# Performance work log

Measured on AMD Instinct MI355X. Metric: run time of the kernel, lower is better.

Reference implementation:

```python
import jax, jax.numpy as jnp
import numpy as np

E, C, D, F = 8, 2048, 2048, 8192  # experts, capacity/expert, d_model, d_ff

def setup_inputs() -> dict:
    key = jax.random.key(0)
    ks = jax.random.split(key, 5)
    s_in = 1.0 / np.sqrt(D)
    s_h = 1.0 / np.sqrt(F)
    return {
        "inputs": jax.random.normal(ks[0], (1, E * C, D), dtype=jnp.float32),
        "w1": jax.random.normal(ks[1], (E, D, F), dtype=jnp.float32) * s_in,
        "b1": jax.random.normal(ks[2], (E, F), dtype=jnp.float32) * 0.01,
        "w2": jax.random.normal(ks[3], (E, F, D), dtype=jnp.float32) * s_h,
        "b2": jax.random.normal(ks[4], (E, D), dtype=jnp.float32) * 0.01,
    }

def reference(inputs, w1, b1, w2, b2):
    # inputs: [G, E*C, D]; chunk along dim=1 == reshape to [G, E, C, D]
    G, T, d = inputs.shape
    x = inputs.reshape(G, E, T // E, d)
    # grouped FFN: per-expert Linear -> GELU(exact, torch default) -> Linear
    h = jnp.einsum('gecd,edf->gecf', x, w1) + b1[None, :, None, :]
    h = jax.nn.gelu(h, approximate=False)
    y = jnp.einsum('gecf,efd->gecd', h, w2) + b2[None, :, None, :]
    # torch.cat(expert_outputs, dim=1) == reshape back
    return y.reshape(G, T, d)
```

## Files before the change

kernel.cpp:

```cpp
#include <hip/hip_runtime.h>
#include <hip/hip_bf16.h>


#define E_ 8
#define C_ 2048
#define D_ 2048
#define F_ 8192

typedef short bf16x8 __attribute__((ext_vector_type(8)));
typedef float f32x4  __attribute__((ext_vector_type(4)));

__device__ inline unsigned short f2bf(float f) {
    unsigned u = __float_as_uint(f);
    u += 0x7fffu + ((u >> 16) & 1u);
    return (unsigned short)(u >> 16);
}

__device__ inline float gelu_fast(float x) {
    float z = 0.7978845608028654f * (x + 0.044715f * x * x * x);
    float e = __expf(-2.0f * fabsf(z));
    float t = (1.0f - e) / (1.0f + e);
    t = copysignf(t, z);
    return 0.5f * x * (1.0f + t);
}

__device__ inline void gload_lds16(const void* g, void* l) {
    __builtin_amdgcn_global_load_lds(
        (const __attribute__((address_space(1))) void*)g,
        (__attribute__((address_space(3))) void*)l, 16, 0, 0);
}

__global__ __launch_bounds__(256) void cvt_kernel(
    const float* __restrict__ in, unsigned short* __restrict__ out, long n4)
{
    long i = (long)blockIdx.x * 256 + threadIdx.x;
    if (i >= n4) return;
    float4 v = ((const float4*)in)[i];
    union { unsigned short u[4]; uint2 q; } r;
    r.u[0] = f2bf(v.x); r.u[1] = f2bf(v.y); r.u[2] = f2bf(v.z); r.u[3] = f2bf(v.w);
    ((uint2*)out)[i] = r.q;
}

__global__ __launch_bounds__(256) void transpose_cvt(
    const float* __restrict__ in, unsigned short* __restrict__ out,
    int R, int Cc, int RT, int CT)
{
    __shared__ float lds[64][65];
    int bx = blockIdx.x;
    int e  = bx / (RT * CT);
    int rem = bx % (RT * CT);
    int rt = rem / CT, ct = rem % CT;
    const float* ine = in + (long)e * R * Cc;
    unsigned short* oute = out + (long)e * R * Cc;
    long r0 = (long)rt * 64, c0 = (long)ct * 64;
    int t = threadIdx.x;

    int lr = t >> 4, lc = t & 15;
#pragma unroll
    for (int ii = 0; ii < 4; ++ii) {
        int r = lr + ii * 16;
        float4 v = *(const float4*)(ine + (r0 + r) * Cc + c0 + lc * 4);
        lds[r][lc * 4 + 0] = v.x; lds[r][lc * 4 + 1] = v.y;
        lds[r][lc * 4 + 2] = v.z; lds[r][lc * 4 + 3] = v.w;
    }
    __syncthreads();

    int nl = t >> 3, kv = t & 7;
#pragma unroll
    for (int ii = 0; ii < 2; ++ii) {
        int n = nl + ii * 32;
        union { unsigned short u[8]; uint4 q; } r;
#pragma unroll
        for (int j = 0; j < 8; ++j) r.u[j] = f2bf(lds[kv * 8 + j][n]);
        *(uint4*)(oute + (c0 + n) * R + r0 + kv * 8) = r.q;
    }
}

#define REG_A0 0
#define REG_A1 16384
#define REG_B0 32768
#define REG_B1 49152
#define SLOT_B 65536

#define MFMA16(d, a, b) d = __builtin_amdgcn_mfma_f32_16x16x32_bf16(a, b, d, 0, 0, 0)
#define CHECKPOINT8() do { \
    asm volatile("s_waitcnt vmcnt(8)" ::: "memory"); \
    __builtin_amdgcn_s_barrier(); } while (0)

template <bool GELU, bool OUT_BF16>
__global__ __launch_bounds__(512, 2) void gemm2p(
    const unsigned short* __restrict__ A,
    const unsigned short* __restrict__ Bt,
    const float* __restrict__ bias,
    void* __restrict__ Cout,
    int M, int N, int K,
    long strideAe, long strideBe, long strideCe, int biasStride)
{
    extern __shared__ char ldsb[];

    constexpr int BM = 256, BN = 256, BK = 64, GRP = 4;
    int MT = M / BM, NT = N / BN;
    int per = MT * NT;
    int nwg = gridDim.x;
    int bid = blockIdx.x;
    int tile = (nwg % 8 == 0) ? (bid & 7) * (nwg >> 3) + (bid >> 3) : bid;
    int e = tile / per, s = tile % per;
    int ng  = s / (MT * GRP);
    int r2  = s % (MT * GRP);
    int mt  = r2 >> 2;
    int nt  = ng * GRP + (r2 & 3);

    const unsigned short* Ae = A  + (long)e * strideAe + (long)mt * BM * K;
    const unsigned short* Be = Bt + (long)e * strideBe + (long)nt * BN * K;

    int tid = threadIdx.x, lane = tid & 63, wid = tid >> 6;
    int wr = wid >> 2, wc = wid & 3;

    int g0 = wid * 128 + lane, g1 = g0 + 64;
    long sOff0, sOff1; int sDst0, sDst1;
    { int row = g0 >> 2, col = g0 & 3, sw = col ^ ((row >> 1) & 3);
      sOff0 = (long)row * K + sw * 8; sDst0 = g0 * 16; }
    { int row = g1 >> 2, col = g1 & 3, sw = col ^ ((row >> 1) & 3);
      sOff1 = (long)row * K + sw * 8; sDst1 = g1 * 16; }

    auto stage_region = [&](const unsigned short* base, int ktile, int kreg, int dstByte) {
        long k0 = (long)ktile * BK + kreg * 32;
        gload_lds16(base + sOff0 + k0, ldsb + dstByte + sDst0);
        gload_lds16(base + sOff1 + k0, ldsb + dstByte + sDst1);
    };

    f32x4 acc[8][4] = {};
    int KT = K / BK;

    int rbaseA = wr * 128 + (lane & 15);
    int rbaseB = wc * 64  + (lane & 15);
    int kq = lane >> 4;
    int baseA = rbaseA * 64 + ((kq ^ ((rbaseA >> 1) & 3)) << 4);
    int baseB = REG_B0 + rbaseB * 64 + ((kq ^ ((rbaseB >> 1) & 3)) << 4);

    stage_region(Ae, 0, 0, REG_A0);
    stage_region(Be, 0, 0, REG_B0);
    stage_region(Ae, 0, 1, REG_A1);
    stage_region(Be, 0, 1, REG_B1);
    stage_region(Ae, 1, 0, SLOT_B + REG_A0);
    stage_region(Be, 1, 0, SLOT_B + REG_B0);
    CHECKPOINT8();

    for (int T = 0; T < KT; ++T) {
        int so = (T & 1) * SLOT_B;
        const char* pA = ldsb + so + baseA;
        const char* pB = ldsb + so + baseB;
        int k1 = (T + 1 < KT) ? T + 1 : KT - 1;
        int k2 = (T + 2 < KT) ? T + 2 : KT - 1;
        int so1 = (k1 & 1) * SLOT_B;
        int so2 = (k2 & 1) * SLOT_B;

        bf16x8 a0[8], b0[4];
#pragma unroll
        for (int n = 0; n < 4; ++n) b0[n] = *(const bf16x8*)(pB + n * 1024);
#pragma unroll
        for (int m = 0; m < 8; ++m) a0[m] = *(const bf16x8*)(pA + m * 1024);
        stage_region(Ae, k1, 1, so1 + REG_A1);
        stage_region(Be, k1, 1, so1 + REG_B1);
#pragma unroll
        for (int m = 0; m < 8; ++m)
#pragma unroll
            for (int n = 0; n < 4; ++n)
                MFMA16(acc[m][n], a0[m], b0[n]);
        CHECKPOINT8();

        bf16x8 a1[8], b1[4];
#pragma unroll
        for (int n = 0; n < 4; ++n) b1[n] = *(const bf16x8*)(pB + 16384 + n * 1024);
#pragma unroll
        for (int m = 0; m < 8; ++m) a1[m] = *(const bf16x8*)(pA + 16384 + m * 1024);
        stage_region(Ae, k2, 0, so2 + REG_A0);
        stage_region(Be, k2, 0, so2 + REG_B0);
#pragma unroll
        for (int m = 0; m < 8; ++m)
#pragma unroll
            for (int n = 0; n < 4; ++n)
                MFMA16(acc[m][n], a1[m], b1[n]);
        CHECKPOINT8();
    }

    asm volatile("s_waitcnt vmcnt(0)" ::: "memory");

    const float* be = bias + (long)e * biasStride + nt * BN;
    long cBase = (long)e * strideCe + ((long)mt * BM) * N + (long)nt * BN;
#pragma unroll
    for (int m = 0; m < 8; ++m) {
#pragma unroll
        for (int n = 0; n < 4; ++n) {
            int col = wc * 64 + n * 16 + (lane & 15);
            float bv = be[col];
#pragma unroll
            for (int j = 0; j < 4; ++j) {
                int row = wr * 128 + m * 16 + (lane >> 4) * 4 + j;
                float v = acc[m][n][j] + bv;
                if (GELU) v = gelu_fast(v);
                long idx = cBase + (long)row * N + col;
                if (OUT_BF16) ((unsigned short*)Cout)[idx] = f2bf(v);
                else          ((float*)Cout)[idx] = v;
            }
        }
    }
}

extern "C" void kernel_launch(void* const* d_in, const int* in_sizes, int n_in,
                              void* d_out, int out_size, void* d_ws, size_t ws_size,
                              hipStream_t stream)
{
    const float* x  = (const float*)d_in[0];
    const float* w1 = (const float*)d_in[1];
    const float* b1 = (const float*)d_in[2];
    const float* w2 = (const float*)d_in[3];
    const float* b2 = (const float*)d_in[4];
    float* out = (float*)d_out;

    (void)hipFuncSetAttribute((const void*)gemm2p<true, true>,
                              hipFuncAttributeMaxDynamicSharedMemorySize, 131072);
    (void)hipFuncSetAttribute((const void*)gemm2p<false, false>,
                              hipFuncAttributeMaxDynamicSharedMemorySize, 131072);

    const long CD = (long)C_ * D_;
    const long DF = (long)D_ * F_;
    const long CF = (long)C_ * F_;
    const long perExpertElems = CD + 2 * DF + CF;
    long ceMax = (long)(ws_size / ((size_t)perExpertElems * 2));
    int CE = (int)(ceMax < 1 ? 1 : (ceMax > E_ ? E_ : ceMax));

    unsigned short* xb  = (unsigned short*)d_ws;
    unsigned short* w1t = xb  + (long)CE * CD;
    unsigned short* w2t = w1t + (long)CE * DF;
    unsigned short* h   = w2t + (long)CE * DF;

    for (int e0 = 0; e0 < E_; e0 += CE) {
        int ce = (E_ - e0) < CE ? (E_ - e0) : CE;

        long n4 = (long)ce * CD / 4;
        cvt_kernel<<<(int)((n4 + 255) / 256), 256, 0, stream>>>(
            x + (long)e0 * CD, xb, n4);

        transpose_cvt<<<ce * (D_ / 64) * (F_ / 64), 256, 0, stream>>>(
            w1 + (long)e0 * DF, w1t, D_, F_, D_ / 64, F_ / 64);

        transpose_cvt<<<ce * (F_ / 64) * (D_ / 64), 256, 0, stream>>>(
            w2 + (long)e0 * DF, w2t, F_, D_, F_ / 64, D_ / 64);

        gemm2p<true, true><<<ce * (C_ / 256) * (F_ / 256), 512, 131072, stream>>>(
            xb, w1t, b1 + (long)e0 * F_, (void*)h,
            C_, F_, D_, CD, DF, CF, F_);

        gemm2p<false, false><<<ce * (C_ / 256) * (D_ / 256), 512, 131072, stream>>>(
            h, w2t, b2 + (long)e0 * D_, (void*)(out + (long)e0 * CD),
            C_, D_, F_, CF, DF, CD, D_);
    }
}
```

Before: 1.359 ms.

## Load B operand fragments directly from global into registers, bypassing LDS

```diff
diff --git a/kernel.cpp b/kernel.cpp
--- a/kernel.cpp
+++ b/kernel.cpp
@@ -76,15 +76,12 @@
     }
 }
 
-#define REG_A0 0
 #define REG_A1 16384
-#define REG_B0 32768
-#define REG_B1 49152
-#define SLOT_B 65536
+#define SLOT_B 32768
 
 #define MFMA16(d, a, b) d = __builtin_amdgcn_mfma_f32_16x16x32_bf16(a, b, d, 0, 0, 0)
-#define CHECKPOINT8() do { \
-    asm volatile("s_waitcnt vmcnt(8)" ::: "memory"); \
+#define CHECKPOINT(N) do { \
+    asm volatile("s_waitcnt vmcnt(" #N ")" ::: "memory"); \
     __builtin_amdgcn_s_barrier(); } while (0)
 
 template <bool GELU, bool OUT_BF16>
@@ -96,7 +93,7 @@
     int M, int N, int K,
     long strideAe, long strideBe, long strideCe, int biasStride)
 {
-    extern __shared__ char ldsb[];
+    __shared__ char ldsb[2 * SLOT_B];
 
     constexpr int BM = 256, BN = 256, BK = 64, GRP = 4;
     int MT = M / BM, NT = N / BN;
@@ -123,65 +120,65 @@
     { int row = g1 >> 2, col = g1 & 3, sw = col ^ ((row >> 1) & 3);
       sOff1 = (long)row * K + sw * 8; sDst1 = g1 * 16; }
 
-    auto stage_region = [&](const unsigned short* base, int ktile, int kreg, int dstByte) {
+    auto stage_A = [&](int ktile, int kreg, int dstByte) {
         long k0 = (long)ktile * BK + kreg * 32;
-        gload_lds16(base + sOff0 + k0, ldsb + dstByte + sDst0);
-        gload_lds16(base + sOff1 + k0, ldsb + dstByte + sDst1);
+        gload_lds16(Ae + sOff0 + k0, ldsb + dstByte + sDst0);
+        gload_lds16(Ae + sOff1 + k0, ldsb + dstByte + sDst1);
     };
+
+    const unsigned short* bPtr[4];
+#pragma unroll
+    for (int n = 0; n < 4; ++n)
+        bPtr[n] = Be + (long)(wc * 64 + n * 16 + (lane & 15)) * K + (lane >> 4) * 8;
 
     f32x4 acc[8][4] = {};
     int KT = K / BK;
 
     int rbaseA = wr * 128 + (lane & 15);
-    int rbaseB = wc * 64  + (lane & 15);
     int kq = lane >> 4;
     int baseA = rbaseA * 64 + ((kq ^ ((rbaseA >> 1) & 3)) << 4);
-    int baseB = REG_B0 + rbaseB * 64 + ((kq ^ ((rbaseB >> 1) & 3)) << 4);
-
-    stage_region(Ae, 0, 0, REG_A0);
-    stage_region(Be, 0, 0, REG_B0);
-    stage_region(Ae, 0, 1, REG_A1);
-    stage_region(Be, 0, 1, REG_B1);
-    stage_region(Ae, 1, 0, SLOT_B + REG_A0);
-    stage_region(Be, 1, 0, SLOT_B + REG_B0);
-    CHECKPOINT8();
+
+    bf16x8 bA[4], bB[4];
+    stage_A(0, 0, 0);
+    stage_A(0, 1, REG_A1);
+#pragma unroll
+    for (int n = 0; n < 4; ++n) bA[n] = *(const bf16x8*)(bPtr[n]);
+    stage_A(1, 0, SLOT_B);
+    CHECKPOINT(8);
 
     for (int T = 0; T < KT; ++T) {
         int so = (T & 1) * SLOT_B;
         const char* pA = ldsb + so + baseA;
-        const char* pB = ldsb + so + baseB;
         int k1 = (T + 1 < KT) ? T + 1 : KT - 1;
         int k2 = (T + 2 < KT) ? T + 2 : KT - 1;
-        int so1 = (k1 & 1) * SLOT_B;
-        int so2 = (k2 & 1) * SLOT_B;
-
-        bf16x8 a0[8], b0[4];
-#pragma unroll
-        for (int n = 0; n < 4; ++n) b0[n] = *(const bf16x8*)(pB + n * 1024);
+
+        bf16x8 a0[8];
 #pragma unroll
         for (int m = 0; m < 8; ++m) a0[m] = *(const bf16x8*)(pA + m * 1024);
-        stage_region(Ae, k1, 1, so1 + REG_A1);
-        stage_region(Be, k1, 1, so1 + REG_B1);
+#pragma unroll
+        for (int n = 0; n < 4; ++n)
+            bB[n] = *(const bf16x8*)(bPtr[n] + (long)T * BK + 32);
+        stage_A(k1, 1, ((k1 & 1) * SLOT_B) + REG_A1);
 #pragma unroll
         for (int m = 0; m < 8; ++m)
 #pragma unroll
             for (int n = 0; n < 4; ++n)
-                MFMA16(acc[m][n], a0[m], b0[n]);
-        CHECKPOINT8();
-
-        bf16x8 a1[8], b1[4];
-#pragma unroll
-        for (int n = 0; n < 4; ++n) b1[n] = *(const bf16x8*)(pB + 16384 + n * 1024);
-#pragma unroll
-        for (int m = 0; m < 8; ++m) a1[m] = *(const bf16x8*)(pA + 16384 + m * 1024);
-        stage_region(Ae, k2, 0, so2 + REG_A0);
-        stage_region(Be, k2, 0, so2 + REG_B0);
+                MFMA16(acc[m][n], a0[m], bA[n]);
+        CHECKPOINT(12);
+
+        bf16x8 a1[8];
+#pragma unroll
+        for (int m = 0; m < 8; ++m) a1[m] = *(const bf16x8*)(pA + REG_A1 + m * 1024);
+#pragma unroll
+        for (int n = 0; n < 4; ++n)
+            bA[n] = *(const bf16x8*)(bPtr[n] + (long)k1 * BK);
+        stage_A(k2, 0, (k2 & 1) * SLOT_B);
 #pragma unroll
         for (int m = 0; m < 8; ++m)
 #pragma unroll
             for (int n = 0; n < 4; ++n)
-                MFMA16(acc[m][n], a1[m], b1[n]);
-        CHECKPOINT8();
+                MFMA16(acc[m][n], a1[m], bB[n]);
+        CHECKPOINT(12);
     }
 
     asm volatile("s_waitcnt vmcnt(0)" ::: "memory");
@@ -218,11 +215,6 @@
     const float* b2 = (const float*)d_in[4];
     float* out = (float*)d_out;
 
-    (void)hipFuncSetAttribute((const void*)gemm2p<true, true>,
-                              hipFuncAttributeMaxDynamicSharedMemorySize, 131072);
-    (void)hipFuncSetAttribute((const void*)gemm2p<false, false>,
-                              hipFuncAttributeMaxDynamicSharedMemorySize, 131072);
-
     const long CD = (long)C_ * D_;
     const long DF = (long)D_ * F_;
     const long CF = (long)C_ * F_;
@@ -248,11 +240,11 @@
         transpose_cvt<<<ce * (F_ / 64) * (D_ / 64), 256, 0, stream>>>(
             w2 + (long)e0 * DF, w2t, F_, D_, F_ / 64, D_ / 64);
 
-        gemm2p<true, true><<<ce * (C_ / 256) * (F_ / 256), 512, 131072, stream>>>(
+        gemm2p<true, true><<<ce * (C_ / 256) * (F_ / 256), 512, 0, stream>>>(
             xb, w1t, b1 + (long)e0 * F_, (void*)h,
             C_, F_, D_, CD, DF, CF, F_);
 
-        gemm2p<false, false><<<ce * (C_ / 256) * (D_ / 256), 512, 131072, stream>>>(
+        gemm2p<false, false><<<ce * (C_ / 256) * (D_ / 256), 512, 0, stream>>>(
             h, w2t, b2 + (long)e0 * D_, (void*)(out + (long)e0 * CD),
             C_, D_, F_, CF, DF, CD, D_);
     }
```

New measurement: 1.742 ms. +28.2%, slower.
